# Optimization experiments

Hardware: AMD Instinct MI355X
Metric: run time of the kernel (lower is better)

The kernel has to match this reference:

```python
import jax, jax.numpy as jnp
import numpy as np

FRAME = 320; SHIFT = 160; FDIM = 256; HDIM = 256; NCLS = 101
EPS_GLN = 1e-5


def _frame_idx(N):
    # same pad rule as torch get_frames/ola
    pad = (N // SHIFT - 1) * SHIFT + FRAME - N
    T = (N + pad - FRAME) // SHIFT + 1
    idx = jnp.arange(T)[:, None] * SHIFT + jnp.arange(FRAME)[None, :]  # [T, FRAME]
    return idx, pad


def setup_inputs() -> dict:
    key = jax.random.key(0)
    ks = jax.random.split(key, 16)
    B, LSIG, LAUX = 32, 160000, 64000
    T_AUX = 400  # frames in a 64000-sample anchor
    T_IN = 1000
    init = lambda k, sh, fan: (jax.random.normal(k, sh, jnp.float32) / np.sqrt(fan)).astype(jnp.float32)
    d = {}
    d['input'] = jax.random.normal(ks[0], (B, LSIG), jnp.float32)
    d['anchor'] = jax.random.normal(ks[1], (B, LAUX), jnp.float32)
    d['aux_len'] = jax.random.randint(ks[2], (B,), 50, T_AUX + 1)
    d['input_len'] = jax.random.randint(ks[3], (B,), T_IN // 2, T_IN + 1)
    d['in_w'] = init(ks[4], (FRAME, FDIM), FRAME); d['in_b'] = jnp.zeros((FDIM,), jnp.float32)
    d['out_w'] = init(ks[5], (FDIM, FRAME), FDIM); d['out_b'] = jnp.zeros((FRAME,), jnp.float32)
    d['gln_g'] = jnp.ones((FDIM,), jnp.float32); d['gln_b'] = jnp.zeros((FDIM,), jnp.float32)
    d['ecapa_w'] = init(ks[6], (FDIM, HDIM), FDIM); d['ecapa_b'] = jnp.zeros((HDIM,), jnp.float32)
    d['att_w1'] = init(ks[7], (3 * HDIM, HDIM), 3 * HDIM); d['att_b1'] = jnp.zeros((HDIM,), jnp.float32)
    d['attbn_g'] = jnp.ones((HDIM,), jnp.float32); d['attbn_b'] = jnp.zeros((HDIM,), jnp.float32)
    d['att_w2'] = init(ks[8], (HDIM, HDIM), HDIM); d['att_b2'] = jnp.zeros((HDIM,), jnp.float32)
    d['bn5_g'] = jnp.ones((2 * HDIM,), jnp.float32); d['bn5_b'] = jnp.zeros((2 * HDIM,), jnp.float32)
    d['fc6_w'] = init(ks[9], (2 * HDIM, FDIM), 2 * HDIM); d['fc6_b'] = jnp.zeros((FDIM,), jnp.float32)
    d['bn6_g'] = jnp.ones((FDIM,), jnp.float32); d['bn6_b'] = jnp.zeros((FDIM,), jnp.float32)
    d['cls_w'] = init(ks[10], (FDIM, NCLS), FDIM); d['cls_b'] = jnp.zeros((NCLS,), jnp.float32)
    d['arn_w1'] = init(ks[11], (4, FDIM, FDIM), FDIM)
    d['arn_w2'] = init(ks[12], (4, FDIM, FDIM), FDIM)
    d['arn_b'] = jnp.zeros((4, FDIM), jnp.float32)
    return d


def _forward(input, anchor, aux_len, input_len, in_w, in_b, out_w, out_b, gln_g, gln_b,
             ecapa_w, ecapa_b, att_w1, att_b1, attbn_g, attbn_b, att_w2, att_b2,
             bn5_g, bn5_b, fc6_w, fc6_b, bn6_g, bn6_b, cls_w, cls_b, arn_w1, arn_w2, arn_b):
    B, LSIG = input.shape
    fin_idx, pad_in = _frame_idx(LSIG)
    frames = jnp.pad(input, ((0, 0), (0, pad_in)))[:, fin_idx]        # [B, Tin, FRAME]
    aux_idx, pad_a = _frame_idx(anchor.shape[1])
    aux_frames = jnp.pad(anchor, ((0, 0), (0, pad_a)))[:, aux_idx]    # [B, Ta, FRAME]

    out = frames @ in_w + in_b                                        # [B, Tin, F]
    aux = aux_frames @ in_w + in_b                                    # [B, Ta, F]
    Ta = aux.shape[1]
    mask = (jnp.arange(Ta)[None, :] < aux_len[:, None]).astype(out.dtype)[:, :, None]  # [B,Ta,1]

    # per-sample GlobalLayerNorm over (valid time, feature) -- replaces python batch loop
    cnt = (aux_len.astype(out.dtype) * FDIM)[:, None, None]
    mean = jnp.sum(aux * mask, (1, 2), keepdims=True) / cnt
    var = jnp.sum(((aux - mean) ** 2) * mask, (1, 2), keepdims=True) / cnt
    auxn = (gln_g * (aux - mean) / jnp.sqrt(var + EPS_GLN) + gln_b) * mask

    # ECAPA res-block stand-in: pointwise conv F->H + ReLU (kernel-1, causal-safe)
    h = jax.nn.relu(auxn @ ecapa_w + ecapa_b) * mask                  # [B, Ta, H]

    # per-sample global stats over valid frames (torch.var is unbiased)
    n = aux_len.astype(out.dtype)[:, None]
    m_t = jnp.sum(h * mask, 1) / n                                    # [B, H]
    v_t = jnp.sum((((h - m_t[:, None, :]) * mask) ** 2), 1) / (n - 1.0)
    s_t = jnp.sqrt(jnp.maximum(v_t, 1e-4))
    gcat = jnp.concatenate([h,
                            jnp.broadcast_to(m_t[:, None, :], h.shape),
                            jnp.broadcast_to(s_t[:, None, :], h.shape)], -1)  # [B,Ta,3H]

    # attention layer: conv1(k=1) -> ReLU -> BN(eval) -> tanh -> conv2(k=1) -> masked softmax over time
    a = jax.nn.relu(gcat @ att_w1 + att_b1)
    a = jnp.tanh(a * attbn_g + attbn_b)
    logits = a @ att_w2 + att_b2
    logits = jnp.where(mask > 0, logits, -1e9)
    w = jax.nn.softmax(logits, axis=1)                                # [B, Ta, H]

    mu = jnp.sum(h * w, 1)                                            # [B, H]
    sg = jnp.sqrt(jnp.maximum(jnp.sum(h * h * w, 1) - mu * mu, 1e-4))
    emb = jnp.concatenate([mu, sg], -1)                               # [B, 2H]
    emb = emb * bn5_g + bn5_b
    emb = emb @ fc6_w + fc6_b
    emb = emb * bn6_g + bn6_b                                         # [B, F]

    nrm = emb / jnp.maximum(jnp.linalg.norm(emb, axis=-1, keepdims=True), 1e-12)
    classify_out = nrm @ cls_w + cls_b                                # [B, 101]

    # 4 ARN blocks (stand-in): residual fusion of frame features with speaker embedding
    for i in range(4):
        out = out + jnp.tanh(out @ arn_w1[i] + (emb @ arn_w2[i])[:, None, :] + arn_b[i])

    out = out @ out_w + out_b                                         # [B, Tin, FRAME]

    # OLA (fold + fold-of-ones denominator)
    flat = fin_idx.reshape(-1)
    Lpad = LSIG + pad_in
    sig = jnp.zeros((B, Lpad), out.dtype).at[:, flat].add(out.reshape(B, -1))
    den = jnp.zeros((Lpad,), out.dtype).at[flat].add(1.0)
    return sig[:, :LSIG] / den[None, :LSIG], classify_out


def reference(input, anchor, aux_len, input_len, in_w, in_b, out_w, out_b, gln_g, gln_b,
              ecapa_w, ecapa_b, att_w1, att_b1, attbn_g, attbn_b, att_w2, att_b2,
              bn5_g, bn5_b, fc6_w, fc6_b, bn6_g, bn6_b, cls_w, cls_b, arn_w1, arn_w2, arn_b):
    return _forward(input, anchor, aux_len, input_len, in_w, in_b, out_w, out_b, gln_g, gln_b,
                    ecapa_w, ecapa_b, att_w1, att_b1, attbn_g, attbn_b, att_w2, att_b2,
                    bn5_g, bn5_b, fc6_w, fc6_b, bn6_g, bn6_b, cls_w, cls_b, arn_w1, arn_w2, arn_b)
```

## Files before the change

### kernel.cpp

```cpp
#include <hip/hip_runtime.h>
#include <math.h>

typedef __attribute__((ext_vector_type(4))) float f32x4;
typedef __attribute__((ext_vector_type(8))) short short8;
typedef __attribute__((ext_vector_type(4))) short bf16x4;

__device__ __forceinline__ short f2bf(float f) {
    unsigned u = __builtin_bit_cast(unsigned, f);
    u += 0x7FFFu + ((u >> 16) & 1u);
    return (short)(u >> 16);
}
__device__ __forceinline__ float bf2f(short s) {
    unsigned u = ((unsigned)(unsigned short)s) << 16;
    return __builtin_bit_cast(float, u);
}
__device__ __forceinline__ short8 pack8(const float* x) {
    short8 r;
    #pragma unroll
    for (int i = 0; i < 8; ++i) r[i] = f2bf(x[i]);
    return r;
}
__device__ __forceinline__ void load16(const float* p, float* x) {
    const float4* q = (const float4*)p;
    #pragma unroll
    for (int i = 0; i < 4; ++i) {
        float4 v = q[i];
        x[i*4+0] = v.x; x[i*4+1] = v.y; x[i*4+2] = v.z; x[i*4+3] = v.w;
    }
}
__device__ __forceinline__ float fast_tanh(float x) {
    float cx = fminf(fmaxf(x, -9.f), 9.f);
    float e = __expf(2.f * cx);
    return (e - 1.f) / (e + 1.f);
}

__global__ __launch_bounds__(256) void convert_wt_k(
    const float* __restrict__ in_w, const float* __restrict__ ecapa_w,
    const float* __restrict__ att_w1, const float* __restrict__ att_w2,
    const float* __restrict__ arn_w1, const float* __restrict__ out_w,
    const float* __restrict__ gln_g, short* __restrict__ WT)
{
    int id = blockIdx.x * 256 + threadIdx.x;
    if (id < 81920) { int n = id / 320, k = id - n * 320; WT[id] = f2bf(in_w[k * 256 + n]); return; }
    id -= 81920;
    if (id < 65536) { int n = id >> 8, k = id & 255; WT[81920 + (n << 8) + k] = f2bf(gln_g[k] * ecapa_w[k * 256 + n]); return; }
    id -= 65536;
    if (id < 65536) { int n = id >> 8, k = id & 255; WT[147456 + (n << 8) + k] = f2bf(att_w1[k * 256 + n]); return; }
    id -= 65536;
    if (id < 65536) { int n = id >> 8, k = id & 255; WT[212992 + (n << 8) + k] = f2bf(att_w2[k * 256 + n]); return; }
    id -= 65536;
    if (id < 262144) {
        int i = id >> 16, r = id & 65535, n = r >> 8, k = r & 255;
        WT[278528 + id] = f2bf(arn_w1[i * 65536 + k * 256 + n]); return;
    }
    id -= 262144;
    if (id < 98304) {
        int n = id >> 8, k = id & 255;
        WT[540672 + id] = (n < 320) ? f2bf(out_w[k * 320 + n]) : (short)0; return;
    }
}

__global__ __launch_bounds__(256) void glnuv_k(const float* __restrict__ ecapa_w,
    const float* __restrict__ gln_g, const float* __restrict__ gln_b,
    const float* __restrict__ ecapa_b, float* __restrict__ uArr, float* __restrict__ vArr)
{
    int n = threadIdx.x;
    float u = 0.f, v = 0.f;
    #pragma unroll 8
    for (int k = 0; k < 256; ++k) {
        float w = ecapa_w[k * 256 + n];
        u = fmaf(gln_g[k], w, u);
        v = fmaf(gln_b[k], w, v);
    }
    uArr[n] = u;
    vArr[n] = v + ecapa_b[n];
}

template<int AMODE, int EPI, int TPB, int OUTBF>
__global__ __launch_bounds__(256) void mfma_gemm_k(
    const float* __restrict__ Asrc, const short* __restrict__ WT,
    const float* __restrict__ bias, void* __restrict__ Cv,
    const float* __restrict__ rowvec,
    const float* __restrict__ ng0, const float* __restrict__ ng1,
    const float* __restrict__ stat0, const float* __restrict__ stat1,
    const int* __restrict__ lens,
    int K, int N, int Lsig)
{
    __shared__ short As[128 * 32];
    __shared__ short Bs[128 * 32];
    const int tid = threadIdx.x;
    const int n0 = blockIdx.x * 128, m0 = blockIdx.y * 128;
    const int rl = tid >> 1, kh = tid & 1;
    const int lane = tid & 63, w = tid >> 6;
    const int wm = w >> 1, wn = w & 1;
    const int lr = lane & 15, ls = lane >> 4;

    const int arow = m0 + rl;
    const float* aptr;
    int tt = 0;
    if (AMODE == 0) {
        aptr = Asrc + (long)arow * K;
    } else {
        int b = arow / TPB; tt = arow - b * TPB;
        aptr = Asrc + (long)b * Lsig + 160 * tt;
    }
    const short* bsrc = WT + (long)(n0 + rl) * K;

    const int s0 = (2 * kh) ^ (rl & 3), s1 = (2 * kh + 1) ^ (rl & 3);
    short* aw0 = &As[rl * 32 + s0 * 8]; short* aw1 = &As[rl * 32 + s1 * 8];
    short* bw0 = &Bs[rl * 32 + s0 * 8]; short* bw1 = &Bs[rl * 32 + s1 * 8];
    const int rco = (ls ^ (lr & 3)) * 8;

    f32x4 acc[4][4] = {};
    float x[16];
    short8 blo, bhi;

    {
        const int kk = kh * 16;
        if (AMODE == 0) {
            load16(aptr + kk, x);
        } else {
            int base = 160 * tt + kk;
            if (base + 15 < Lsig) load16(aptr + kk, x);
            else {
                #pragma unroll
                for (int e = 0; e < 16; ++e) x[e] = (base + e < Lsig) ? aptr[kk + e] : 0.f;
            }
        }
        blo = *(const short8*)(bsrc + kk);
        bhi = *(const short8*)(bsrc + kk + 8);
    }

    for (int k0 = 0; k0 < K; k0 += 32) {
        *(short8*)aw0 = pack8(x);
        *(short8*)aw1 = pack8(x + 8);
        *(short8*)bw0 = blo;
        *(short8*)bw1 = bhi;
        __syncthreads();
        if (k0 + 32 < K) {
            const int kk = k0 + 32 + kh * 16;
            if (AMODE == 0) {
                load16(aptr + kk, x);
            } else {
                int base = 160 * tt + kk;
                if (base + 15 < Lsig) load16(aptr + kk, x);
                else {
                    #pragma unroll
                    for (int e = 0; e < 16; ++e) x[e] = (base + e < Lsig) ? aptr[kk + e] : 0.f;
                }
            }
            blo = *(const short8*)(bsrc + kk);
            bhi = *(const short8*)(bsrc + kk + 8);
        }
        short8 af[4], bfr[4];
        #pragma unroll
        for (int f = 0; f < 4; ++f) {
            af[f]  = *(const short8*)&As[(wm * 64 + f * 16 + lr) * 32 + rco];
            bfr[f] = *(const short8*)&Bs[(wn * 64 + f * 16 + lr) * 32 + rco];
        }
        #pragma unroll
        for (int fr = 0; fr < 4; ++fr)
            #pragma unroll
            for (int fc = 0; fc < 4; ++fc)
                acc[fr][fc] = __builtin_amdgcn_mfma_f32_16x16x32_bf16(bfr[fc], af[fr], acc[fr][fc], 0, 0, 0);
        __syncthreads();
    }

    #pragma unroll
    for (int fr = 0; fr < 4; ++fr) {
        const int row = m0 + wm * 64 + fr * 16 + lr;
        int bb = 0, tloc = 0;
        if (EPI != 0) { bb = row / TPB; tloc = row - bb * TPB; }
        float mean = 0.f, rstd = 0.f; int lenb = 0;
        if (EPI == 5) { mean = stat0[bb]; rstd = stat1[bb]; lenb = lens[bb]; }
        #pragma unroll
        for (int fc = 0; fc < 4; ++fc) {
            const int col = n0 + wn * 64 + fc * 16 + ls * 4;
            if (col >= N) continue;
            f32x4 a = acc[fr][fc];
            float4 r;
            if (EPI == 0) {
                float4 bv = *(const float4*)(bias + col);
                r.x = a[0] + bv.x; r.y = a[1] + bv.y; r.z = a[2] + bv.z; r.w = a[3] + bv.w;
            } else if (EPI == 2) {
                float4 rvv = *(const float4*)(rowvec + bb * 256 + col);
                float4 g0 = *(const float4*)(ng0 + col);
                float4 g1 = *(const float4*)(ng1 + col);
                r.x = fast_tanh(fmaxf(a[0] + rvv.x, 0.f) * g0.x + g1.x);
                r.y = fast_tanh(fmaxf(a[1] + rvv.y, 0.f) * g0.y + g1.y);
                r.z = fast_tanh(fmaxf(a[2] + rvv.z, 0.f) * g0.z + g1.z);
                r.w = fast_tanh(fmaxf(a[3] + rvv.w, 0.f) * g0.w + g1.w);
            } else {
                float4 uu = *(const float4*)(ng0 + col);
                float4 vv = *(const float4*)(ng1 + col);
                bool val = tloc < lenb;
                r.x = val ? fmaxf(rstd * (a[0] - mean * uu.x) + vv.x, 0.f) : 0.f;
                r.y = val ? fmaxf(rstd * (a[1] - mean * uu.y) + vv.y, 0.f) : 0.f;
                r.z = val ? fmaxf(rstd * (a[2] - mean * uu.z) + vv.z, 0.f) : 0.f;
                r.w = val ? fmaxf(rstd * (a[3] - mean * uu.w) + vv.w, 0.f) : 0.f;
            }
            if (OUTBF) {
                bf16x4 o; o[0] = f2bf(r.x); o[1] = f2bf(r.y); o[2] = f2bf(r.z); o[3] = f2bf(r.w);
                *(bf16x4*)((short*)Cv + (long)row * N + col) = o;
            } else {
                *(float4*)((float*)Cv + (long)row * N + col) = r;
            }
        }
    }
}

__global__ __launch_bounds__(512) void arn_fused_k(
    const short* __restrict__ o0b, const short* __restrict__ WT_arn,
    const short* __restrict__ WT_out, const float* __restrict__ out_b,
    const float* __restrict__ arnvec, float* __restrict__ y)
{
    __shared__ short Tb[2][128 * 256];
    const int tid = threadIdx.x;
    const int m0 = blockIdx.x * 128;
    const int lane = tid & 63, w = tid >> 6;
    const int wm = w >> 2, wn = w & 3;
    const int lr = lane & 15, ls = lane >> 4;

    {
        int row = tid >> 2, q = (tid & 3) * 8;
        const short* src = o0b + (long)(m0 + row) * 256 + q * 8;
        #pragma unroll
        for (int s = 0; s < 8; ++s) {
            short8 v = *(const short8*)(src + s * 8);
            int slot = q + s;
            *(short8*)&Tb[0][row * 256 + ((slot ^ (row & 7)) << 3)] = v;
        }
    }
    __syncthreads();

    f32x4 r[4][4];
    #pragma unroll
    for (int fr = 0; fr < 4; ++fr) {
        int row = wm * 64 + fr * 16 + lr;
        #pragma unroll
        for (int fc = 0; fc < 4; ++fc) {
            int col = wn * 64 + fc * 16 + ls * 4;
            int slot = col >> 3, off = col & 7;
            bf16x4 v = *(const bf16x4*)&Tb[0][row * 256 + ((slot ^ (row & 7)) << 3) + off];
            r[fr][fc][0] = bf2f(v[0]); r[fr][fc][1] = bf2f(v[1]);
            r[fr][fc][2] = bf2f(v[2]); r[fr][fc][3] = bf2f(v[3]);
        }
    }

    int cur = 0;
    for (int i = 0; i < 4; ++i) {
        const short* Wl = WT_arn + (long)i * 65536;
        const float* rv = arnvec + (long)i * 8192;
        f32x4 acc[4][4] = {};
        #pragma unroll
        for (int ks = 0; ks < 8; ++ks) {
            short8 af[4], bq[4];
            #pragma unroll
            for (int fr = 0; fr < 4; ++fr) {
                int row = wm * 64 + fr * 16 + lr;
                int slot = ks * 4 + ls;
                af[fr] = *(const short8*)&Tb[cur][row * 256 + ((slot ^ (row & 7)) << 3)];
            }
            #pragma unroll
            for (int fc = 0; fc < 4; ++fc) {
                int n = wn * 64 + fc * 16 + lr;
                bq[fc] = *(const short8*)(Wl + n * 256 + ks * 32 + ls * 8);
            }
            #pragma unroll
            for (int fr = 0; fr < 4; ++fr)
                #pragma unroll
                for (int fc = 0; fc < 4; ++fc)
                    acc[fr][fc] = __builtin_amdgcn_mfma_f32_16x16x32_bf16(bq[fc], af[fr], acc[fr][fc], 0, 0, 0);
        }
        #pragma unroll
        for (int fr = 0; fr < 4; ++fr) {
            int rowl = wm * 64 + fr * 16 + lr;
            int bb = (m0 + rowl) / 1000;
            #pragma unroll
            for (int fc = 0; fc < 4; ++fc) {
                int col = wn * 64 + fc * 16 + ls * 4;
                float4 rvv = *(const float4*)(rv + bb * 256 + col);
                f32x4 a = acc[fr][fc];
                r[fr][fc][0] += fast_tanh(a[0] + rvv.x);
                r[fr][fc][1] += fast_tanh(a[1] + rvv.y);
                r[fr][fc][2] += fast_tanh(a[2] + rvv.z);
                r[fr][fc][3] += fast_tanh(a[3] + rvv.w);
                bf16x4 o;
                o[0] = f2bf(r[fr][fc][0]); o[1] = f2bf(r[fr][fc][1]);
                o[2] = f2bf(r[fr][fc][2]); o[3] = f2bf(r[fr][fc][3]);
                int slot = col >> 3, off = col & 7;
                *(bf16x4*)&Tb[cur ^ 1][rowl * 256 + ((slot ^ (rowl & 7)) << 3) + off] = o;
            }
        }
        cur ^= 1;
        __syncthreads();
    }

    f32x4 pacc[5][4] = {};
    #pragma unroll
    for (int ks = 0; ks < 8; ++ks) {
        short8 af[4];
        #pragma unroll
        for (int fr = 0; fr < 4; ++fr) {
            int row = wm * 64 + fr * 16 + lr;
            int slot = ks * 4 + ls;
            af[fr] = *(const short8*)&Tb[cur][row * 256 + ((slot ^ (row & 7)) << 3)];
        }
        #pragma unroll
        for (int fc = 0; fc < 5; ++fc) {
            int n = wn * 80 + fc * 16 + lr;
            short8 bq = *(const short8*)(WT_out + n * 256 + ks * 32 + ls * 8);
            #pragma unroll
            for (int fr = 0; fr < 4; ++fr)
                pacc[fc][fr] = __builtin_amdgcn_mfma_f32_16x16x32_bf16(bq, af[fr], pacc[fc][fr], 0, 0, 0);
        }
    }
    #pragma unroll
    for (int fc = 0; fc < 5; ++fc) {
        #pragma unroll
        for (int fr = 0; fr < 4; ++fr) {
            int row = m0 + wm * 64 + fr * 16 + lr;
            int cb = wn * 80 + fc * 16 + ls * 4;
            float4 ob = *(const float4*)(out_b + cb);
            f32x4 a = pacc[fc][fr];
            float4 o;
            o.x = a[0] + ob.x; o.y = a[1] + ob.y; o.z = a[2] + ob.z; o.w = a[3] + ob.w;
            *(float4*)(y + (long)row * 320 + cb) = o;
        }
    }
}

__global__ __launch_bounds__(256) void gln_part_k(const float* __restrict__ aux,
    const int* __restrict__ lens, float* __restrict__ part)
{
    int b = blockIdx.x, p = blockIdx.y, tid = threadIdx.x;
    int len = lens[b];
    int t0 = p * 25, t1 = min(len, t0 + 25);
    const float4* src = (const float4*)(aux + (long)b * 400 * 256);
    float s = 0.f, ss = 0.f;
    for (int i = t0 * 64 + tid; i < t1 * 64; i += 256) {
        float4 v = src[i];
        s += v.x + v.y + v.z + v.w;
        ss += v.x*v.x + v.y*v.y + v.z*v.z + v.w*v.w;
    }
    for (int off = 32; off; off >>= 1) { s += __shfl_down(s, off); ss += __shfl_down(ss, off); }
    __shared__ float l1[4], l2[4];
    if ((tid & 63) == 0) { l1[tid >> 6] = s; l2[tid >> 6] = ss; }
    __syncthreads();
    if (tid == 0) {
        part[b * 16 + p]       = l1[0] + l1[1] + l1[2] + l1[3];
        part[512 + b * 16 + p] = l2[0] + l2[1] + l2[2] + l2[3];
    }
}

__global__ __launch_bounds__(512) void gln_comb_k(const float* __restrict__ part,
    const int* __restrict__ lens, float* __restrict__ meanA, float* __restrict__ rstdA)
{
    __shared__ float s1[32][16], s2[32][16];
    int tid = threadIdx.x, b = tid >> 4, p = tid & 15;
    s1[b][p] = part[b * 16 + p];
    s2[b][p] = part[512 + b * 16 + p];
    __syncthreads();
    if (tid < 32) {
        float s = 0.f, ss = 0.f;
        for (int q = 0; q < 16; ++q) { s += s1[tid][q]; ss += s2[tid][q]; }
        float cnt = (float)lens[tid] * 256.f;
        float mean = s / cnt;
        float var = ss / cnt - mean * mean;
        meanA[tid] = mean;
        rstdA[tid] = 1.0f / sqrtf(var + 1e-5f);
    }
}

__global__ __launch_bounds__(256) void stats_part_k(const float* __restrict__ h,
    const int* __restrict__ lens, float* __restrict__ part)
{
    int b = blockIdx.x, p = blockIdx.y, c = threadIdx.x;
    int len = lens[b];
    int t0 = p * 50, t1 = min(len, t0 + 50);
    const float* hp = h + ((long)b * 400 + t0) * 256 + c;
    float s = 0.f, ss = 0.f;
    for (int t = 0; t < t1 - t0; ++t) { float v = hp[(long)t * 256]; s += v; ss = fmaf(v, v, ss); }
    part[((long)b * 8 + p) * 256 + c] = s;
    part[65536 + ((long)b * 8 + p) * 256 + c] = ss;
}

__global__ __launch_bounds__(256) void stats_comb_k(const float* __restrict__ part,
    const int* __restrict__ lens, const float* __restrict__ att_w1,
    const float* __restrict__ att_b1, float* __restrict__ attbias)
{
    int b = blockIdx.x, c = threadIdx.x;
    float s = 0.f, ss = 0.f;
    #pragma unroll
    for (int p = 0; p < 8; ++p) {
        s += part[((long)b * 8 + p) * 256 + c];
        ss += part[65536 + ((long)b * 8 + p) * 256 + c];
    }
    float n = (float)lens[b];
    float m = s / n;
    float var = (ss - n * m * m) / (n - 1.0f);
    float sd = sqrtf(fmaxf(var, 1e-4f));
    __shared__ float mS[256], sS[256];
    mS[c] = m; sS[c] = sd;
    __syncthreads();
    float a0 = att_b1[c], a1 = 0.f;
    #pragma unroll 4
    for (int k = 0; k < 256; ++k) {
        a0 = fmaf(mS[k], att_w1[(256 + k) * 256 + c], a0);
        a1 = fmaf(sS[k], att_w1[(512 + k) * 256 + c], a1);
    }
    attbias[b * 256 + c] = a0 + a1;
}

__global__ __launch_bounds__(256) void softmax_part_k(const float* __restrict__ logits,
    const float* __restrict__ h, const int* __restrict__ lens, float* __restrict__ part)
{
    int b = blockIdx.x, p = blockIdx.y, c = threadIdx.x;
    int len = lens[b];
    int t0 = p * 50, t1 = min(len, t0 + 50);
    int nt = t1 - t0;
    const float* lp = logits + ((long)b * 400 + t0) * 256 + c;
    const float* hp = h + ((long)b * 400 + t0) * 256 + c;
    float mx = -1e30f;
    for (int t = 0; t < nt; ++t) mx = fmaxf(mx, lp[(long)t * 256]);
    float den = 0.f, mu = 0.f, m2 = 0.f;
    for (int t = 0; t < nt; ++t) {
        float e = __expf(lp[(long)t * 256] - mx);
        float hv = hp[(long)t * 256];
        den += e;
        mu = fmaf(e, hv, mu);
        m2 = fmaf(e * hv, hv, m2);
    }
    long o = ((long)b * 8 + p) * 256 + c;
    part[o] = mx; part[o + 65536] = den; part[o + 131072] = mu; part[o + 196608] = m2;
}

__global__ __launch_bounds__(256) void softmax_comb_k(const float* __restrict__ part,
    const float* __restrict__ bn5g, const float* __restrict__ bn5b, float* __restrict__ e5)
{
    int b = blockIdx.x, c = threadIdx.x;
    float mx[8], M = -1e30f;
    #pragma unroll
    for (int p = 0; p < 8; ++p) { mx[p] = part[((long)b * 8 + p) * 256 + c]; M = fmaxf(M, mx[p]); }
    float den = 0.f, mu = 0.f, m2 = 0.f;
    #pragma unroll
    for (int p = 0; p < 8; ++p) {
        long o = ((long)b * 8 + p) * 256 + c;
        float sc = __expf(mx[p] - M);
        den = fmaf(part[o + 65536], sc, den);
        mu  = fmaf(part[o + 131072], sc, mu);
        m2  = fmaf(part[o + 196608], sc, m2);
    }
    mu /= den; m2 /= den;
    float sg = sqrtf(fmaxf(m2 - mu * mu, 1e-4f));
    e5[b * 512 + c]       = mu * bn5g[c] + bn5b[c];
    e5[b * 512 + 256 + c] = sg * bn5g[256 + c] + bn5b[256 + c];
}

__global__ __launch_bounds__(1024) void emb_k(const float* __restrict__ e5,
    const float* __restrict__ fc6w, const float* __restrict__ fc6b,
    const float* __restrict__ bn6g, const float* __restrict__ bn6b,
    const float* __restrict__ clsw, const float* __restrict__ clsb,
    float* __restrict__ classify, float* __restrict__ embG)
{
    int b = blockIdx.x, tid = threadIdx.x;
    int g = tid >> 8, c = tid & 255;
    __shared__ float es[512], embS[256], fP[4][256], red[4], cP[8][128];
    __shared__ float invS;
    if (tid < 512) es[tid] = e5[b * 512 + tid];
    __syncthreads();
    float acc = 0.f;
    for (int k = g * 128; k < g * 128 + 128; ++k)
        acc = fmaf(es[k], fc6w[k * 256 + c], acc);
    fP[g][c] = acc;
    __syncthreads();
    if (g == 0) {
        float e = fP[0][c] + fP[1][c] + fP[2][c] + fP[3][c] + fc6b[c];
        float eb = e * bn6g[c] + bn6b[c];
        embS[c] = eb;
        embG[b * 256 + c] = eb;
    }
    __syncthreads();
    if (tid < 256) {
        float sq = embS[tid] * embS[tid];
        for (int off = 32; off; off >>= 1) sq += __shfl_down(sq, off);
        if ((tid & 63) == 0) red[tid >> 6] = sq;
    }
    __syncthreads();
    if (tid == 0) invS = 1.0f / fmaxf(sqrtf(red[0] + red[1] + red[2] + red[3]), 1e-12f);
    __syncthreads();
    int g8 = tid >> 7, c7 = tid & 127;
    float a = 0.f;
    if (c7 < 101)
        for (int k = g8 * 32; k < g8 * 32 + 32; ++k)
            a = fmaf(embS[k], clsw[k * 101 + c7], a);
    cP[g8][c7] = a;
    __syncthreads();
    if (g8 == 0 && c7 < 101) {
        float ssum = 0.f;
        #pragma unroll
        for (int q = 0; q < 8; ++q) ssum += cP[q][c7];
        classify[b * 101 + c7] = ssum * invS + clsb[c7];
    }
}

__global__ __launch_bounds__(256) void arnvec_k(const float* __restrict__ embG,
    const float* __restrict__ arnw2, const float* __restrict__ arnb,
    float* __restrict__ arnvec)
{
    int i = blockIdx.x >> 5, b = blockIdx.x & 31, c = threadIdx.x;
    __shared__ float e[256];
    e[c] = embG[b * 256 + c];
    __syncthreads();
    const float* wp = arnw2 + (long)i * 65536;
    float a0 = arnb[i * 256 + c], a1 = 0.f;
    #pragma unroll 4
    for (int k = 0; k < 256; k += 2) {
        a0 = fmaf(e[k], wp[(long)k * 256 + c], a0);
        a1 = fmaf(e[k + 1], wp[(long)(k + 1) * 256 + c], a1);
    }
    arnvec[((long)i * 32 + b) * 256 + c] = a0 + a1;
}

__global__ __launch_bounds__(256) void ola_k(const float* __restrict__ y, float* __restrict__ out)
{
    int gidx = blockIdx.x * 256 + threadIdx.x;
    if (gidx >= 32 * 160000) return;
    int b = gidx / 160000;
    int p = gidx - b * 160000;
    int t0 = p / 160;
    int k0 = p - t0 * 160;
    const float* yb = y + (long)b * 1000 * 320;
    float v = yb[(long)t0 * 320 + k0];
    if (t0 > 0) { v += yb[(long)(t0 - 1) * 320 + k0 + 160]; v *= 0.5f; }
    out[gidx] = v;
}

extern "C" void kernel_launch(void* const* d_in, const int* in_sizes, int n_in,
                              void* d_out, int out_size, void* d_ws, size_t ws_size,
                              hipStream_t stream)
{
    (void)in_sizes; (void)n_in; (void)out_size; (void)ws_size;
    const float* input   = (const float*)d_in[0];
    const float* anchor  = (const float*)d_in[1];
    const int*   aux_len = (const int*)d_in[2];
    const float* in_w    = (const float*)d_in[4];
    const float* in_b    = (const float*)d_in[5];
    const float* out_w   = (const float*)d_in[6];
    const float* out_b   = (const float*)d_in[7];
    const float* gln_g   = (const float*)d_in[8];
    const float* gln_b   = (const float*)d_in[9];
    const float* ecapa_w = (const float*)d_in[10];
    const float* ecapa_b = (const float*)d_in[11];
    const float* att_w1  = (const float*)d_in[12];
    const float* att_b1  = (const float*)d_in[13];
    const float* attbn_g = (const float*)d_in[14];
    const float* attbn_b = (const float*)d_in[15];
    const float* att_w2  = (const float*)d_in[16];
    const float* att_b2  = (const float*)d_in[17];
    const float* bn5_g   = (const float*)d_in[18];
    const float* bn5_b   = (const float*)d_in[19];
    const float* fc6_w   = (const float*)d_in[20];
    const float* fc6_b   = (const float*)d_in[21];
    const float* bn6_g   = (const float*)d_in[22];
    const float* bn6_b   = (const float*)d_in[23];
    const float* cls_w   = (const float*)d_in[24];
    const float* cls_b   = (const float*)d_in[25];
    const float* arn_w1  = (const float*)d_in[26];
    const float* arn_w2  = (const float*)d_in[27];
    const float* arn_b   = (const float*)d_in[28];

    float* out_sig = (float*)d_out;
    float* out_cls = out_sig + (long)32 * 160000;

    float* ws = (float*)d_ws;
    short* o0b    = (short*)ws;
    float* aux    = ws + 4096000;
    float* logits = aux;
    float* h      = ws + 7372800;
    float* a2     = ws + 10649600;
    float* y      = ws + 13926400;
    float* glnpart = y;
    float* stpart  = y + 4096;
    float* smpart  = y + 140000;
    short* WT     = (short*)(ws + 24166400);
    float* smalls = ws + 24485888;
    float* meanA   = smalls;
    float* rstdA   = smalls + 32;
    float* attbias = smalls + 64;
    float* e5      = smalls + 64 + 8192;
    float* arnvec  = e5 + 16384;
    float* uArr    = arnvec + 32768;
    float* vArr    = uArr + 256;
    float* embG    = vArr + 256;

    short* WT_in  = WT;
    short* WT_ec  = WT + 81920;
    short* WT_a1  = WT + 147456;
    short* WT_a2  = WT + 212992;
    short* WT_arn = WT + 278528;
    short* WT_out = WT + 540672;

    dim3 blk(256);

    convert_wt_k<<<dim3(2496), blk, 0, stream>>>(in_w, ecapa_w, att_w1, att_w2, arn_w1, out_w, gln_g, WT);
    glnuv_k<<<dim3(1), blk, 0, stream>>>(ecapa_w, gln_g, gln_b, ecapa_b, uArr, vArr);

    mfma_gemm_k<1, 0, 1000, 1><<<dim3(2, 250), blk, 0, stream>>>(input, WT_in, in_b, o0b,
        nullptr, nullptr, nullptr, nullptr, nullptr, nullptr, 320, 256, 160000);
    mfma_gemm_k<1, 0, 400, 0><<<dim3(2, 100), blk, 0, stream>>>(anchor, WT_in, in_b, aux,
        nullptr, nullptr, nullptr, nullptr, nullptr, nullptr, 320, 256, 64000);
    gln_part_k<<<dim3(32, 16), blk, 0, stream>>>(aux, aux_len, glnpart);
    gln_comb_k<<<dim3(1), dim3(512), 0, stream>>>(glnpart, aux_len, meanA, rstdA);
    mfma_gemm_k<0, 5, 400, 0><<<dim3(2, 100), blk, 0, stream>>>(aux, WT_ec, nullptr, h,
        nullptr, uArr, vArr, meanA, rstdA, aux_len, 256, 256, 0);
    stats_part_k<<<dim3(32, 8), blk, 0, stream>>>(h, aux_len, stpart);
    stats_comb_k<<<dim3(32), blk, 0, stream>>>(stpart, aux_len, att_w1, att_b1, attbias);
    mfma_gemm_k<0, 2, 400, 0><<<dim3(2, 100), blk, 0, stream>>>(h, WT_a1, nullptr, a2,
        attbias, attbn_g, attbn_b, nullptr, nullptr, nullptr, 256, 256, 0);
    mfma_gemm_k<0, 0, 400, 0><<<dim3(2, 100), blk, 0, stream>>>(a2, WT_a2, att_b2, logits,
        nullptr, nullptr, nullptr, nullptr, nullptr, nullptr, 256, 256, 0);
    softmax_part_k<<<dim3(32, 8), blk, 0, stream>>>(logits, h, aux_len, smpart);
    softmax_comb_k<<<dim3(32), blk, 0, stream>>>(smpart, bn5_g, bn5_b, e5);
    emb_k<<<dim3(32), dim3(1024), 0, stream>>>(e5, fc6_w, fc6_b, bn6_g, bn6_b, cls_w, cls_b,
                                               out_cls, embG);
    arnvec_k<<<dim3(128), blk, 0, stream>>>(embG, arn_w2, arn_b, arnvec);
    arn_fused_k<<<dim3(250), dim3(512), 0, stream>>>(o0b, WT_arn, WT_out, out_b, arnvec, y);
    ola_k<<<dim3(20000), blk, 0, stream>>>(y, out_sig);
}
```

Measured before the change: 390.0 us.

## Shrink ARN fused tile to 64 rows single-buffered and vectorize OLA

The fused ARN kernel now processes 64-row tiles with 256 threads and a single LDS buffer, adding a barrier before the in-place writeback, and launches 500 blocks instead of 250. This spreads work across more CUs and lowers LDS per block so several blocks can be resident at once, at the cost of an extra sync per layer and reloading the weight fragments for twice as many blocks. The OLA kernel is also vectorized to handle four samples per thread with float4 loads and stores.

```diff
diff --git a/kernel.cpp b/kernel.cpp
--- a/kernel.cpp
+++ b/kernel.cpp
@@ -209,16 +209,15 @@
     }
 }
 
-__global__ __launch_bounds__(512) void arn_fused_k(
+__global__ __launch_bounds__(256, 3) void arn_fused_k(
     const short* __restrict__ o0b, const short* __restrict__ WT_arn,
     const short* __restrict__ WT_out, const float* __restrict__ out_b,
     const float* __restrict__ arnvec, float* __restrict__ y)
 {
-    __shared__ short Tb[2][128 * 256];
+    __shared__ short Tb[64 * 256];
     const int tid = threadIdx.x;
-    const int m0 = blockIdx.x * 128;
-    const int lane = tid & 63, w = tid >> 6;
-    const int wm = w >> 2, wn = w & 3;
+    const int m0 = blockIdx.x * 64;
+    const int lane = tid & 63, wn = tid >> 6;
     const int lr = lane & 15, ls = lane >> 4;
 
     {
@@ -228,7 +227,7 @@
         for (int s = 0; s < 8; ++s) {
             short8 v = *(const short8*)(src + s * 8);
             int slot = q + s;
-            *(short8*)&Tb[0][row * 256 + ((slot ^ (row & 7)) << 3)] = v;
+            *(short8*)&Tb[row * 256 + ((slot ^ (row & 7)) << 3)] = v;
         }
     }
     __syncthreads();
@@ -236,18 +235,17 @@
     f32x4 r[4][4];
     #pragma unroll
     for (int fr = 0; fr < 4; ++fr) {
-        int row = wm * 64 + fr * 16 + lr;
+        int row = fr * 16 + lr;
         #pragma unroll
         for (int fc = 0; fc < 4; ++fc) {
             int col = wn * 64 + fc * 16 + ls * 4;
             int slot = col >> 3, off = col & 7;
-            bf16x4 v = *(const bf16x4*)&Tb[0][row * 256 + ((slot ^ (row & 7)) << 3) + off];
+            bf16x4 v = *(const bf16x4*)&Tb[row * 256 + ((slot ^ (row & 7)) << 3) + off];
             r[fr][fc][0] = bf2f(v[0]); r[fr][fc][1] = bf2f(v[1]);
             r[fr][fc][2] = bf2f(v[2]); r[fr][fc][3] = bf2f(v[3]);
         }
     }
 
-    int cur = 0;
     for (int i = 0; i < 4; ++i) {
         const short* Wl = WT_arn + (long)i * 65536;
         const float* rv = arnvec + (long)i * 8192;
@@ -257,9 +255,9 @@
             short8 af[4], bq[4];
             #pragma unroll
             for (int fr = 0; fr < 4; ++fr) {
-                int row = wm * 64 + fr * 16 + lr;
+                int row = fr * 16 + lr;
                 int slot = ks * 4 + ls;
-                af[fr] = *(const short8*)&Tb[cur][row * 256 + ((slot ^ (row & 7)) << 3)];
+                af[fr] = *(const short8*)&Tb[row * 256 + ((slot ^ (row & 7)) << 3)];
             }
             #pragma unroll
             for (int fc = 0; fc < 4; ++fc) {
@@ -272,9 +270,10 @@
                 for (int fc = 0; fc < 4; ++fc)
                     acc[fr][fc] = __builtin_amdgcn_mfma_f32_16x16x32_bf16(bq[fc], af[fr], acc[fr][fc], 0, 0, 0);
         }
+        __syncthreads();
         #pragma unroll
         for (int fr = 0; fr < 4; ++fr) {
-            int rowl = wm * 64 + fr * 16 + lr;
+            int rowl = fr * 16 + lr;
             int bb = (m0 + rowl) / 1000;
             #pragma unroll
             for (int fc = 0; fc < 4; ++fc) {
@@ -289,22 +288,21 @@
                 o[0] = f2bf(r[fr][fc][0]); o[1] = f2bf(r[fr][fc][1]);
                 o[2] = f2bf(r[fr][fc][2]); o[3] = f2bf(r[fr][fc][3]);
                 int slot = col >> 3, off = col & 7;
-                *(bf16x4*)&Tb[cur ^ 1][rowl * 256 + ((slot ^ (rowl & 7)) << 3) + off] = o;
+                *(bf16x4*)&Tb[rowl * 256 + ((slot ^ (rowl & 7)) << 3) + off] = o;
             }
         }
-        cur ^= 1;
         __syncthreads();
     }
 
-    f32x4 pacc[5][4] = {};
+    f32x4 pacc[4][5] = {};
     #pragma unroll
     for (int ks = 0; ks < 8; ++ks) {
         short8 af[4];
         #pragma unroll
         for (int fr = 0; fr < 4; ++fr) {
-            int row = wm * 64 + fr * 16 + lr;
+            int row = fr * 16 + lr;
             int slot = ks * 4 + ls;
-            af[fr] = *(const short8*)&Tb[cur][row * 256 + ((slot ^ (row & 7)) << 3)];
+            af[fr] = *(const short8*)&Tb[row * 256 + ((slot ^ (row & 7)) << 3)];
         }
         #pragma unroll
         for (int fc = 0; fc < 5; ++fc) {
@@ -312,17 +310,17 @@
             short8 bq = *(const short8*)(WT_out + n * 256 + ks * 32 + ls * 8);
             #pragma unroll
             for (int fr = 0; fr < 4; ++fr)
-                pacc[fc][fr] = __builtin_amdgcn_mfma_f32_16x16x32_bf16(bq, af[fr], pacc[fc][fr], 0, 0, 0);
+                pacc[fr][fc] = __builtin_amdgcn_mfma_f32_16x16x32_bf16(bq, af[fr], pacc[fr][fc], 0, 0, 0);
         }
     }
     #pragma unroll
     for (int fc = 0; fc < 5; ++fc) {
         #pragma unroll
         for (int fr = 0; fr < 4; ++fr) {
-            int row = m0 + wm * 64 + fr * 16 + lr;
+            int row = m0 + fr * 16 + lr;
             int cb = wn * 80 + fc * 16 + ls * 4;
             float4 ob = *(const float4*)(out_b + cb);
-            f32x4 a = pacc[fc][fr];
+            f32x4 a = pacc[fr][fc];
             float4 o;
             o.x = a[0] + ob.x; o.y = a[1] + ob.y; o.z = a[2] + ob.z; o.w = a[3] + ob.w;
             *(float4*)(y + (long)row * 320 + cb) = o;
@@ -524,16 +522,22 @@
 
 __global__ __launch_bounds__(256) void ola_k(const float* __restrict__ y, float* __restrict__ out)
 {
-    int gidx = blockIdx.x * 256 + threadIdx.x;
-    if (gidx >= 32 * 160000) return;
-    int b = gidx / 160000;
-    int p = gidx - b * 160000;
+    int g4 = blockIdx.x * 256 + threadIdx.x;
+    if (g4 >= 32 * 40000) return;
+    int b = g4 / 40000;
+    int p = (g4 - b * 40000) * 4;
     int t0 = p / 160;
     int k0 = p - t0 * 160;
     const float* yb = y + (long)b * 1000 * 320;
-    float v = yb[(long)t0 * 320 + k0];
-    if (t0 > 0) { v += yb[(long)(t0 - 1) * 320 + k0 + 160]; v *= 0.5f; }
-    out[gidx] = v;
+    float4 v = *(const float4*)(yb + (long)t0 * 320 + k0);
+    if (t0 > 0) {
+        float4 u = *(const float4*)(yb + (long)(t0 - 1) * 320 + k0 + 160);
+        v.x = (v.x + u.x) * 0.5f;
+        v.y = (v.y + u.y) * 0.5f;
+        v.z = (v.z + u.z) * 0.5f;
+        v.w = (v.w + u.w) * 0.5f;
+    }
+    *(float4*)(out + (long)b * 160000 + p) = v;
 }
 
 extern "C" void kernel_launch(void* const* d_in, const int* in_sizes, int n_in,
@@ -625,6 +629,6 @@
     emb_k<<<dim3(32), dim3(1024), 0, stream>>>(e5, fc6_w, fc6_b, bn6_g, bn6_b, cls_w, cls_b,
                                                out_cls, embG);
     arnvec_k<<<dim3(128), blk, 0, stream>>>(embG, arn_w2, arn_b, arnvec);
-    arn_fused_k<<<dim3(250), dim3(512), 0, stream>>>(o0b, WT_arn, WT_out, out_b, arnvec, y);
-    ola_k<<<dim3(20000), blk, 0, stream>>>(y, out_sig);
-}
+    arn_fused_k<<<dim3(500), blk, 0, stream>>>(o0b, WT_arn, WT_out, out_b, arnvec, y);
+    ola_k<<<dim3(5000), blk, 0, stream>>>(y, out_sig);
+}
```

After: 446.9 us. 14.6% more time.
